# Kernel tuning notes

Hardware: AMD Instinct MI355X
Metric: run time of the kernel (lower is better)

The kernel has to match this reference:

```python
import jax, jax.numpy as jnp
import numpy as np

B, T, D, H, HS, E, K = 8, 1024, 1024, 16, 64, 8, 2
DF = 4 * D


def setup_inputs() -> dict:
    key = jax.random.key(0)
    ks = jax.random.split(key, 16)
    s = 0.02
    return {
        "x": jax.random.normal(ks[0], (B, T, D), jnp.float32),
        "noise": jax.random.normal(ks[1], (B, T, E), jnp.float32),
        # per-head attention projections, stacked over heads [H, D, HS]
        "Wq": jax.random.normal(ks[2], (H, D, HS), jnp.float32) * s,
        "Wk": jax.random.normal(ks[3], (H, D, HS), jnp.float32) * s,
        "Wv": jax.random.normal(ks[4], (H, D, HS), jnp.float32) * s,
        "Wproj": jax.random.normal(ks[5], (D, D), jnp.float32) * s,
        "bproj": jnp.zeros((D,), jnp.float32),
        "ln1_g": jnp.ones((D,), jnp.float32),
        "ln1_b": jnp.zeros((D,), jnp.float32),
        "ln2_g": jnp.ones((D,), jnp.float32),
        "ln2_b": jnp.zeros((D,), jnp.float32),
        # router
        "Wr": jax.random.normal(ks[6], (D, E), jnp.float32) * s,
        "br": jnp.zeros((E,), jnp.float32),
        "Wn": jax.random.normal(ks[7], (D, E), jnp.float32) * s,
        "bn": jnp.zeros((E,), jnp.float32),
        # experts, stacked [E, ...]
        "W1": jax.random.normal(ks[8], (E, D, DF), jnp.float32) * s,
        "b1": jnp.zeros((E, DF), jnp.float32),
        "W2": jax.random.normal(ks[9], (E, DF, D), jnp.float32) * s,
        "b2": jnp.zeros((E, D), jnp.float32),
    }


def _layernorm(x, g, b, eps=1e-5):
    mu = jnp.mean(x, axis=-1, keepdims=True)
    var = jnp.mean(jnp.square(x - mu), axis=-1, keepdims=True)
    return (x - mu) * jax.lax.rsqrt(var + eps) * g + b


def reference(x, noise, Wq, Wk, Wv, Wproj, bproj, ln1_g, ln1_b, ln2_g, ln2_b,
              Wr, br, Wn, bn, W1, b1, W2, b2):
    b_, t_, d_ = x.shape
    # ---- multi-head causal self-attention (dropout = identity, eval mode) ----
    h = _layernorm(x, ln1_g, ln1_b)
    q = jnp.einsum("btd,hdk->bhtk", h, Wq)
    k = jnp.einsum("btd,hdk->bhtk", h, Wk)
    v = jnp.einsum("btd,hdk->bhtk", h, Wv)
    # NOTE: original scales by C**-0.5 with C = n_embed (not head_size)
    score = jnp.einsum("bhqk,bhsk->bhqs", q, k) * (d_ ** -0.5)
    causal = jnp.tril(jnp.ones((t_, t_), bool))
    score = jnp.where(causal, score, -jnp.inf)
    att = jax.nn.softmax(score, axis=-1)
    o = jnp.einsum("bhqs,bhsk->bhqk", att, v)
    o = o.transpose(0, 2, 1, 3).reshape(b_, t_, d_)  # concat heads
    x = x + o @ Wproj + bproj
    # ---- noisy top-k sparse MoE ----
    h2 = _layernorm(x, ln2_g, ln2_b)
    logits = h2 @ Wr + br
    noisy_logits = logits + noise * jax.nn.softplus(h2 @ Wn + bn)
    topv, topi = jax.lax.top_k(noisy_logits, K)          # [B,T,K]
    sel = (topi[..., None] == jnp.arange(E)).any(axis=-2)  # [B,T,E] bool
    sparse = jnp.where(sel, noisy_logits, -jnp.inf)
    gate = jax.nn.softmax(sparse, axis=-1)               # zeros off top-k
    # gate[:,:,e]==0 for unselected experts, so dense sum == sparse dispatch
    moe = jnp.zeros_like(x)
    for e in range(E):
        he = jax.nn.relu(h2 @ W1[e] + b1[e]) @ W2[e] + b2[e]
        moe = moe + gate[..., e:e + 1] * he
    return x + moe
```

## Files before the change

### kernel.cpp

```cpp
#include <hip/hip_runtime.h>
#include <hip/hip_bf16.h>
#include <math.h>

#define NTOK 8192
#define DN   1024
#define HN   16
#define HSN  64
#define EN   8
#define DFN  4096
#define TN   1024
#define NQ   8388608u
#define NPB  144

typedef _Float16 f16x8 __attribute__((ext_vector_type(8)));
typedef _Float16 f16x4 __attribute__((ext_vector_type(4)));
typedef float    f32x4 __attribute__((ext_vector_type(4)));
typedef short    s16x8 __attribute__((ext_vector_type(8)));

#define MFMA_F16(A,B,C)  __builtin_amdgcn_mfma_f32_16x16x32_f16((A),(B),(C),0,0,0)
#define MFMA_BF16(A,B,C) __builtin_amdgcn_mfma_f32_16x16x32_bf16((A),(B),(C),0,0,0)

__device__ __forceinline__ unsigned short f2bf(float f){
  union { float f; unsigned u; } v; v.f = f;
  unsigned r = v.u + 0x7fffu + ((v.u >> 16) & 1u);
  return (unsigned short)(r >> 16);
}
__device__ __forceinline__ void fsplit(float v, _Float16& hi, _Float16& lo){
  hi = (_Float16)v; lo = (_Float16)(v - (float)hi);
}
__device__ __forceinline__ void gload16(const void* g, void* l){
  __builtin_amdgcn_global_load_lds((const __attribute__((address_space(1))) unsigned int*)g,
                                   (__attribute__((address_space(3))) unsigned int*)l, 16, 0, 0);
}
#define BAR() __builtin_amdgcn_s_barrier()
#define VMW_BAR(N) do { \
  asm volatile("s_waitcnt vmcnt(" #N ")" ::: "memory"); \
  __builtin_amdgcn_s_barrier(); \
} while (0)

__global__ __launch_bounds__(128) void ln1_kernel(
    const float* __restrict__ x, const float* __restrict__ g, const float* __restrict__ be,
    unsigned char* __restrict__ aph, unsigned char* __restrict__ apl)
{
  const int row = blockIdx.x;
  const int t = threadIdx.x;
  __shared__ float red[2];
  float4 va = ((const float4*)(x + (size_t)row*DN))[t*2];
  float4 vb = ((const float4*)(x + (size_t)row*DN))[t*2+1];
  float s = va.x+va.y+va.z+va.w + vb.x+vb.y+vb.z+vb.w;
  #pragma unroll
  for (int m = 32; m >= 1; m >>= 1) s += __shfl_xor(s, m);
  if ((t & 63) == 0) red[t >> 6] = s;
  __syncthreads();
  const float mu = (red[0] + red[1]) * (1.0f / DN);
  float e[8] = { va.x-mu, va.y-mu, va.z-mu, va.w-mu, vb.x-mu, vb.y-mu, vb.z-mu, vb.w-mu };
  float s2 = 0.0f;
  #pragma unroll
  for (int i = 0; i < 8; i++) s2 += e[i]*e[i];
  #pragma unroll
  for (int m = 32; m >= 1; m >>= 1) s2 += __shfl_xor(s2, m);
  __syncthreads();
  if ((t & 63) == 0) red[t >> 6] = s2;
  __syncthreads();
  const float var = (red[0] + red[1]) * (1.0f / DN);
  const float rs = 1.0f / sqrtf(var + 1e-5f);
  float4 ga = ((const float4*)g)[t*2], gb = ((const float4*)g)[t*2+1];
  float4 ba = ((const float4*)be)[t*2], bb = ((const float4*)be)[t*2+1];
  float gg[8] = { ga.x,ga.y,ga.z,ga.w, gb.x,gb.y,gb.z,gb.w };
  float bbv[8] = { ba.x,ba.y,ba.z,ba.w, bb.x,bb.y,bb.z,bb.w };
  f16x8 hi8, lo8;
  #pragma unroll
  for (int i = 0; i < 8; i++){
    _Float16 hi, lo; fsplit((e[i]*rs*gg[i] + bbv[i]) * 64.0f, hi, lo);
    hi8[i] = hi; lo8[i] = lo;
  }
  const int pb = row >> 7, r = row & 127, kt = t >> 3, kk8 = t & 7;
  size_t po = ((size_t)(pb*16 + kt))*16384 + r*128 + (size_t)((kk8 ^ (r & 7)) << 4);
  *(f16x8*)(aph + po) = hi8;
  *(f16x8*)(apl + po) = lo8;
}

__global__ __launch_bounds__(256) void wsplit_kernel(
    const float* __restrict__ Wq, const float* __restrict__ Wk, const float* __restrict__ Wv,
    const float* __restrict__ Wp,
    unsigned char* __restrict__ bqh, unsigned char* __restrict__ bql,
    unsigned char* __restrict__ bph, unsigned char* __restrict__ bpl)
{
  int b = blockIdx.x;
  const int t = threadIdx.x;
  const int r = t & 127;
  const int c0 = (t >> 7) * 4;
  if (b < 384){
    int nb = b >> 4, kt = b & 15;
    int n = nb*128 + r;
    int mat = n >> 10, h = (n >> 6) & 15, hs = n & 63;
    const float* W = (mat == 0) ? Wq : ((mat == 1) ? Wk : Wv);
    const float* src = W + (size_t)h*65536 + hs;
    unsigned char* ph = bqh + ((size_t)(nb*16 + kt))*16384 + r*128;
    unsigned char* pl = bql + ((size_t)(nb*16 + kt))*16384 + r*128;
    #pragma unroll
    for (int c = c0; c < c0 + 4; c++){
      int kk8 = c ^ (r & 7);
      f16x8 hi8, lo8;
      #pragma unroll
      for (int j = 0; j < 8; j++){
        _Float16 hi, lo; fsplit(src[(size_t)(kt*64 + kk8*8 + j)*64] * 1024.0f, hi, lo);
        hi8[j] = hi; lo8[j] = lo;
      }
      *(f16x8*)(ph + c*16) = hi8;
      *(f16x8*)(pl + c*16) = lo8;
    }
  } else {
    b -= 384;
    int nb = b >> 4, kt = b & 15;
    int n = nb*128 + r;
    unsigned char* ph = bph + ((size_t)(nb*16 + kt))*16384 + r*128;
    unsigned char* pl = bpl + ((size_t)(nb*16 + kt))*16384 + r*128;
    #pragma unroll
    for (int c = c0; c < c0 + 4; c++){
      int kk8 = c ^ (r & 7);
      f16x8 hi8, lo8;
      #pragma unroll
      for (int j = 0; j < 8; j++){
        _Float16 hi, lo; fsplit(Wp[(size_t)(kt*64 + kk8*8 + j)*DN + n] * 1024.0f, hi, lo);
        hi8[j] = hi; lo8[j] = lo;
      }
      *(f16x8*)(ph + c*16) = hi8;
      *(f16x8*)(pl + c*16) = lo8;
    }
  }
}

__global__ __launch_bounds__(256) void qkv_gemm_kernel(
    const unsigned char* __restrict__ aph, const unsigned char* __restrict__ apl,
    const unsigned char* __restrict__ bqh, const unsigned char* __restrict__ bql,
    _Float16* __restrict__ qkvout)
{
  const int mb = blockIdx.x;
  const int nb = blockIdx.y;
  __shared__ __align__(16) unsigned char As[16384], Bs[16384];
  const int t = threadIdx.x, w = t >> 6, lane = t & 63, lg = lane >> 4, lr = lane & 15;
  const int wr = w >> 1, wc = w & 1;
  f32x4 acc[4][4] = {};
  for (int kp = 0; kp < 48; kp++){
    const int ktl = kp & 15, phse = kp >> 4;
    if (w < 2){
      const unsigned char* srcA = (phse == 1 ? apl : aph) + ((size_t)(mb*16 + ktl))*16384;
      const unsigned char* s2 = srcA + w*8192 + lane*16;
      unsigned char* d = As + w*8192;
      #pragma unroll
      for (int j = 0; j < 8; j++) gload16(s2 + j*1024, d + j*1024);
    } else {
      const unsigned char* srcB = (phse == 2 ? bql : bqh) + ((size_t)(nb*16 + ktl))*16384;
      const unsigned char* s2 = srcB + (w - 2)*8192 + lane*16;
      unsigned char* d = Bs + (w - 2)*8192;
      #pragma unroll
      for (int j = 0; j < 8; j++) gload16(s2 + j*1024, d + j*1024);
    }
    __syncthreads();
    #pragma unroll
    for (int ks = 0; ks < 2; ks++){
      f16x8 a[4], bfr[4];
      #pragma unroll
      for (int f = 0; f < 4; f++){
        int ra = wr*64 + f*16 + lr;
        a[f] = *(const f16x8*)(As + ra*128 + ((ks*64 + lg*16) ^ ((ra & 7) << 4)));
      }
      #pragma unroll
      for (int f = 0; f < 4; f++){
        int rb = wc*64 + f*16 + lr;
        bfr[f] = *(const f16x8*)(Bs + rb*128 + ((ks*64 + lg*16) ^ ((rb & 7) << 4)));
      }
      #pragma unroll
      for (int fm = 0; fm < 4; fm++)
      #pragma unroll
      for (int fn = 0; fn < 4; fn++)
        acc[fm][fn] = MFMA_F16(a[fm], bfr[fn], acc[fm][fn]);
    }
    __syncthreads();
  }
  #pragma unroll
  for (int fm = 0; fm < 4; fm++)
  #pragma unroll
  for (int fn = 0; fn < 4; fn++)
  #pragma unroll
  for (int rr = 0; rr < 4; rr++){
    int m = mb*128 + wr*64 + fm*16 + lg*4 + rr;
    int n = nb*128 + wc*64 + fn*16 + lr;
    int mat = n >> 10, h = (n >> 6) & 15, hs = n & 63;
    int bb = m >> 10, tt = m & 1023;
    _Float16* dsthi = qkvout + (size_t)mat * 2u * NQ;
    _Float16* dstlo = dsthi + NQ;
    size_t oi = (((size_t)(bb*HN + h))*TN + tt)*HSN + hs;
    _Float16 hi, lo; fsplit(acc[fm][fn][rr] * (1.0f/1024.0f), hi, lo);
    dsthi[oi] = hi; dstlo[oi] = lo;
  }
}

__global__ __launch_bounds__(256) void attn_kernel(
    const _Float16* __restrict__ qkv,
    _Float16* __restrict__ ohi_, _Float16* __restrict__ olo_)
{
  const _Float16* qhi = qkv;
  const _Float16* qlo = qkv + NQ;
  const _Float16* khi = qkv + 2u*NQ;
  const _Float16* klo = qkv + 3u*NQ;
  const _Float16* vhi = qkv + 4u*NQ;
  const _Float16* vlo = qkv + 5u*NQ;
  const int qt = blockIdx.x;
  const int bh = blockIdx.y;
  const size_t base = (size_t)bh * TN * HSN;
  const int t = threadIdx.x, wid = t >> 6, lane = t & 63, lg = lane >> 4, lr = lane & 15;
  __shared__ _Float16 Khi[64][72], Klo[64][72], Vthi[64][72], Vtlo[64][72], Phi[64][72], Plo[64][72];
  f16x8 qh[2], ql[2];
  {
    const int qrow = qt*64 + wid*16 + lr;
    const _Float16* qp  = qhi + base + (size_t)qrow*HSN;
    const _Float16* qpl = qlo + base + (size_t)qrow*HSN;
    #pragma unroll
    for (int c = 0; c < 2; c++){
      qh[c] = *(const f16x8*)(qp  + c*32 + lg*8);
      ql[c] = *(const f16x8*)(qpl + c*32 + lg*8);
    }
  }
  f32x4 oacc[4] = {};
  float mrow[4], lsum[4];
  #pragma unroll
  for (int r = 0; r < 4; r++){ mrow[r] = -INFINITY; lsum[r] = 0.0f; }
  const int sr = t >> 2, sc = (t & 3) * 16;
  const float sscale = 1.0f / (4096.0f * 32.0f);
  for (int kvt = 0; kvt <= qt; kvt++){
    {
      const size_t gr = base + (size_t)(kvt*64 + sr)*HSN + sc;
      *(f16x8*)&Khi[sr][sc]     = *(const f16x8*)(khi + gr);
      *(f16x8*)&Khi[sr][sc + 8] = *(const f16x8*)(khi + gr + 8);
      *(f16x8*)&Klo[sr][sc]     = *(const f16x8*)(klo + gr);
      *(f16x8*)&Klo[sr][sc + 8] = *(const f16x8*)(klo + gr + 8);
      f16x8 v0 = *(const f16x8*)(vhi + gr), v1 = *(const f16x8*)(vhi + gr + 8);
      f16x8 w0 = *(const f16x8*)(vlo + gr), w1 = *(const f16x8*)(vlo + gr + 8);
      #pragma unroll
      for (int j = 0; j < 8; j++){
        Vthi[sc + j][sr] = v0[j]; Vthi[sc + 8 + j][sr] = v1[j];
        Vtlo[sc + j][sr] = w0[j]; Vtlo[sc + 8 + j][sr] = w1[j];
      }
    }
    __syncthreads();
    f32x4 sacc[4] = {};
    #pragma unroll
    for (int c = 0; c < 2; c++)
    #pragma unroll
    for (int fn = 0; fn < 4; fn++){
      f16x8 kh = *(const f16x8*)&Khi[fn*16 + lr][c*32 + lg*8];
      f16x8 kl = *(const f16x8*)&Klo[fn*16 + lr][c*32 + lg*8];
      sacc[fn] = MFMA_F16(qh[c], kh, sacc[fn]);
      sacc[fn] = MFMA_F16(qh[c], kl, sacc[fn]);
      sacc[fn] = MFMA_F16(ql[c], kh, sacc[fn]);
    }
    float sv[4][4], pmax[4];
    #pragma unroll
    for (int r = 0; r < 4; r++) pmax[r] = -INFINITY;
    const int qg0 = qt*64 + wid*16 + lg*4;
    #pragma unroll
    for (int fn = 0; fn < 4; fn++)
    #pragma unroll
    for (int r = 0; r < 4; r++){
      float xv = sacc[fn][r] * sscale;
      int kvg = kvt*64 + fn*16 + lr;
      xv = (kvg <= qg0 + r) ? xv : -INFINITY;
      sv[fn][r] = xv;
      pmax[r] = fmaxf(pmax[r], xv);
    }
    #pragma unroll
    for (int r = 0; r < 4; r++){
      #pragma unroll
      for (int m = 1; m < 16; m <<= 1) pmax[r] = fmaxf(pmax[r], __shfl_xor(pmax[r], m));
    }
    float alpha[4], mnew[4], psum[4];
    #pragma unroll
    for (int r = 0; r < 4; r++){
      mnew[r] = fmaxf(mrow[r], pmax[r]);
      alpha[r] = __expf(mrow[r] - mnew[r]);
      psum[r] = 0.0f;
    }
    #pragma unroll
    for (int fn = 0; fn < 4; fn++)
    #pragma unroll
    for (int r = 0; r < 4; r++){
      float p = __expf(sv[fn][r] - mnew[r]);
      psum[r] += p;
      _Float16 hi, lo; fsplit(p * 512.0f, hi, lo);
      Phi[wid*16 + lg*4 + r][fn*16 + lr] = hi;
      Plo[wid*16 + lg*4 + r][fn*16 + lr] = lo;
    }
    #pragma unroll
    for (int r = 0; r < 4; r++){
      #pragma unroll
      for (int m = 1; m < 16; m <<= 1) psum[r] += __shfl_xor(psum[r], m);
      lsum[r] = lsum[r]*alpha[r] + psum[r];
      mrow[r] = mnew[r];
    }
    #pragma unroll
    for (int fn = 0; fn < 4; fn++)
    #pragma unroll
    for (int r = 0; r < 4; r++) oacc[fn][r] *= alpha[r];
    #pragma unroll
    for (int c2 = 0; c2 < 2; c2++){
      f16x8 ph = *(const f16x8*)&Phi[wid*16 + lr][c2*32 + lg*8];
      f16x8 pl = *(const f16x8*)&Plo[wid*16 + lr][c2*32 + lg*8];
      #pragma unroll
      for (int fn = 0; fn < 4; fn++){
        f16x8 vh = *(const f16x8*)&Vthi[fn*16 + lr][c2*32 + lg*8];
        f16x8 vl = *(const f16x8*)&Vtlo[fn*16 + lr][c2*32 + lg*8];
        oacc[fn] = MFMA_F16(ph, vh, oacc[fn]);
        oacc[fn] = MFMA_F16(ph, vl, oacc[fn]);
        oacc[fn] = MFMA_F16(pl, vh, oacc[fn]);
      }
    }
    __syncthreads();
  }
  const int bb = bh >> 4, hh = bh & 15;
  #pragma unroll
  for (int fn = 0; fn < 4; fn++)
  #pragma unroll
  for (int r = 0; r < 4; r++){
    float ov = oacc[fn][r] / (32768.0f * lsum[r]);
    int m = qt*64 + wid*16 + lg*4 + r;
    size_t oi = ((size_t)(bb*TN + m))*DN + hh*HSN + fn*16 + lr;
    _Float16 hi, lo; fsplit(ov * 64.0f, hi, lo);
    ohi_[oi] = hi; olo_[oi] = lo;
  }
}

__global__ __launch_bounds__(256) void proj_gemm_kernel(
    const _Float16* __restrict__ ohi, const _Float16* __restrict__ olo,
    const unsigned char* __restrict__ bph, const unsigned char* __restrict__ bpl,
    const float* __restrict__ x, const float* __restrict__ bproj,
    float* __restrict__ out)
{
  const int mb = blockIdx.x;
  const int nb = blockIdx.y;
  __shared__ __align__(16) unsigned char As[16384], Bs[16384];
  const int t = threadIdx.x, w = t >> 6, lane = t & 63, lg = lane >> 4, lr = lane & 15;
  const int wr = w >> 1, wc = w & 1;
  f32x4 acc[4][4] = {};
  for (int kp = 0; kp < 48; kp++){
    const int ktl = kp & 15, phse = kp >> 4;
    if (w < 2){
      const _Float16* basep = (phse == 1 ? olo : ohi);
      const int rA = w*64 + (lane >> 3);
      const int c = lane & 7;
      unsigned char* d = As + w*8192;
      #pragma unroll
      for (int j = 0; j < 8; j++){
        int r = rA + j*8;
        const unsigned char* s2 = (const unsigned char*)(basep + (size_t)(mb*128 + r)*DN)
                                  + ktl*128 + ((c ^ (r & 7)) << 4);
        gload16(s2, d + j*1024);
      }
    } else {
      const unsigned char* srcB = (phse == 2 ? bpl : bph) + ((size_t)(nb*16 + ktl))*16384;
      const unsigned char* s2 = srcB + (w - 2)*8192 + lane*16;
      unsigned char* d = Bs + (w - 2)*8192;
      #pragma unroll
      for (int j = 0; j < 8; j++) gload16(s2 + j*1024, d + j*1024);
    }
    __syncthreads();
    #pragma unroll
    for (int ks = 0; ks < 2; ks++){
      f16x8 a[4], bfr[4];
      #pragma unroll
      for (int f = 0; f < 4; f++){
        int ra = wr*64 + f*16 + lr;
        a[f] = *(const f16x8*)(As + ra*128 + ((ks*64 + lg*16) ^ ((ra & 7) << 4)));
      }
      #pragma unroll
      for (int f = 0; f < 4; f++){
        int rb = wc*64 + f*16 + lr;
        bfr[f] = *(const f16x8*)(Bs + rb*128 + ((ks*64 + lg*16) ^ ((rb & 7) << 4)));
      }
      #pragma unroll
      for (int fm = 0; fm < 4; fm++)
      #pragma unroll
      for (int fn = 0; fn < 4; fn++)
        acc[fm][fn] = MFMA_F16(a[fm], bfr[fn], acc[fm][fn]);
    }
    __syncthreads();
  }
  #pragma unroll
  for (int fm = 0; fm < 4; fm++)
  #pragma unroll
  for (int fn = 0; fn < 4; fn++)
  #pragma unroll
  for (int rr = 0; rr < 4; rr++){
    int m = mb*128 + wr*64 + fm*16 + lg*4 + rr;
    int n = nb*128 + wc*64 + fn*16 + lr;
    size_t oi = (size_t)m*DN + n;
    out[oi] = x[oi] + acc[fm][fn][rr] * (1.0f/65536.0f) + bproj[n];
  }
}

__global__ __launch_bounds__(256) void router_kernel(
    const float* __restrict__ x1, const float* __restrict__ g, const float* __restrict__ be,
    const float* __restrict__ Wr, const float* __restrict__ br,
    const float* __restrict__ Wn, const float* __restrict__ bn,
    const float* __restrict__ noise, unsigned short* __restrict__ h2bf,
    int* __restrict__ topk_e, float* __restrict__ topk_g, int* __restrict__ counts)
{
  const int token = blockIdx.x;
  const int t = threadIdx.x;
  __shared__ float redsum[4];
  __shared__ float red[64];
  float4 v = ((const float4*)(x1 + (size_t)token * DN))[t];
  float s = v.x + v.y + v.z + v.w;
  #pragma unroll
  for (int m = 32; m >= 1; m >>= 1) s += __shfl_xor(s, m);
  if ((t & 63) == 0) redsum[t >> 6] = s;
  __syncthreads();
  const float mu = (redsum[0] + redsum[1] + redsum[2] + redsum[3]) * (1.0f / DN);
  const float d0 = v.x - mu, d1 = v.y - mu, d2 = v.z - mu, d3 = v.w - mu;
  float s2 = d0*d0 + d1*d1 + d2*d2 + d3*d3;
  #pragma unroll
  for (int m = 32; m >= 1; m >>= 1) s2 += __shfl_xor(s2, m);
  __syncthreads();
  if ((t & 63) == 0) redsum[t >> 6] = s2;
  __syncthreads();
  const float var = (redsum[0] + redsum[1] + redsum[2] + redsum[3]) * (1.0f / DN);
  const float rs = 1.0f / sqrtf(var + 1e-5f);
  float4 gv = ((const float4*)g)[t];
  float4 bv = ((const float4*)be)[t];
  float h0 = d0*rs*gv.x + bv.x, h1v = d1*rs*gv.y + bv.y, h2v = d2*rs*gv.z + bv.z, h3 = d3*rs*gv.w + bv.w;
  ushort4 hb;
  hb.x = f2bf(h0); hb.y = f2bf(h1v); hb.z = f2bf(h2v); hb.w = f2bf(h3);
  *(ushort4*)(h2bf + (size_t)token*DN + t*4) = hb;
  float acc[16];
  const int j = t * 4;
  #pragma unroll
  for (int e = 0; e < 8; e++){
    acc[e]     = h0*Wr[(j+0)*8+e] + h1v*Wr[(j+1)*8+e] + h2v*Wr[(j+2)*8+e] + h3*Wr[(j+3)*8+e];
    acc[8 + e] = h0*Wn[(j+0)*8+e] + h1v*Wn[(j+1)*8+e] + h2v*Wn[(j+2)*8+e] + h3*Wn[(j+3)*8+e];
  }
  #pragma unroll
  for (int q = 0; q < 16; q++){
    #pragma unroll
    for (int m = 32; m >= 1; m >>= 1) acc[q] += __shfl_xor(acc[q], m);
  }
  if ((t & 63) == 0){
    #pragma unroll
    for (int q = 0; q < 16; q++) red[(t >> 6)*16 + q] = acc[q];
  }
  __syncthreads();
  if (t < 16) red[t] = red[t] + red[16 + t] + red[32 + t] + red[48 + t];
  __syncthreads();
  if (t == 0){
    float nz[8];
    #pragma unroll
    for (int e = 0; e < 8; e++){
      float logit = red[e] + br[e];
      float a = red[8 + e] + bn[e];
      float sp = (a > 20.0f) ? a : log1pf(expf(a));
      nz[e] = logit + noise[(size_t)token*EN + e] * sp;
    }
    float v1 = -INFINITY, v2 = -INFINITY; int i1 = 0, i2 = 0;
    #pragma unroll
    for (int e = 0; e < 8; e++){
      float z = nz[e];
      if (z > v1){ v2 = v1; i2 = i1; v1 = z; i1 = e; }
      else if (z > v2){ v2 = z; i2 = e; }
    }
    float e2 = expf(v2 - v1);
    float den = 1.0f + e2;
    topk_e[token*2]     = i1; topk_e[token*2 + 1] = i2;
    topk_g[token*2]     = 1.0f/den; topk_g[token*2 + 1] = e2/den;
    atomicAdd(&counts[i1], 1); atomicAdd(&counts[i2], 1);
  }
}

__global__ void scan_kernel(const int* __restrict__ counts, int* __restrict__ offs)
{
  if (threadIdx.x == 0 && blockIdx.x == 0){
    int a = 0;
    for (int e = 0; e < EN; e++){ offs[e] = a; a += (counts[e] + 255) & ~255; }
  }
}

__global__ __launch_bounds__(256) void scatter_kernel(
    const int* __restrict__ topk_e, const float* __restrict__ topk_g,
    const int* __restrict__ offs, int* __restrict__ fill,
    int* __restrict__ rows, float* __restrict__ grow)
{
  const int token = blockIdx.x*256 + threadIdx.x;
  #pragma unroll
  for (int i = 0; i < 2; i++){
    int e = topk_e[token*2 + i];
    int pos = offs[e] + atomicAdd(&fill[e], 1);
    rows[pos] = token;
    grow[pos] = topk_g[token*2 + i];
  }
}

__global__ __launch_bounds__(256) void wconv_kernel(
    const float* __restrict__ W1, const float* __restrict__ W2,
    unsigned char* __restrict__ w1p, unsigned char* __restrict__ w2p)
{
  int b = blockIdx.x;
  const float* W; unsigned char* pan; int Nd, kt, n;
  if (b < 2048){
    int e = b >> 8, rem = b & 255, nb2 = rem >> 4; kt = rem & 15;
    n = nb2*256 + threadIdx.x;
    W = W1 + (size_t)e * DN * DFN; Nd = DFN;
    pan = w1p + (((size_t)e*32 + (n >> 7))*16 + kt) * 16384;
  } else {
    b -= 2048;
    int e = b >> 8, rem = b & 255, nb2 = rem >> 6; kt = rem & 63;
    n = nb2*256 + threadIdx.x;
    W = W2 + (size_t)e * DFN * DN; Nd = DN;
    pan = w2p + (((size_t)e*8 + (n >> 7))*64 + kt) * 16384;
  }
  const int r = n & 127;
  #pragma unroll
  for (int kk8 = 0; kk8 < 8; kk8++){
    union { unsigned short u[8]; uint4 v; } buf;
    #pragma unroll
    for (int j = 0; j < 8; j++)
      buf.u[j] = f2bf(W[(size_t)(kt*64 + kk8*8 + j)*Nd + n]);
    *(uint4*)(pan + r*128 + ((kk8 ^ (r & 7)) << 4)) = buf.v;
  }
}

__global__ __launch_bounds__(256) void agather_kernel(
    const unsigned short* __restrict__ h2bf, const int* __restrict__ rows,
    unsigned char* __restrict__ apnl)
{
  const int pb = blockIdx.x, kt = blockIdx.y;
  const int t = threadIdx.x;
  const int r = t >> 1, c0 = (t & 1) * 4;
  const int tok = rows[pb*128 + r];
  const unsigned char* src = (const unsigned char*)h2bf + (size_t)tok*2048 + kt*128;
  unsigned char* dst = apnl + ((size_t)pb*16 + kt)*16384 + r*128;
  #pragma unroll
  for (int i = 0; i < 4; i++){
    int c = c0 + i;
    *(uint4*)(dst + ((c ^ (r & 7)) << 4)) = *(const uint4*)(src + c*16);
  }
}

__global__ __launch_bounds__(512, 1) void moe1_kernel(
    const unsigned char* __restrict__ apnl, const unsigned char* __restrict__ w1p,
    const float* __restrict__ b1,
    const int* __restrict__ counts, const int* __restrict__ offs,
    unsigned short* __restrict__ midP)
{
  __shared__ __align__(16) unsigned char As[2][32768], Bs[2][32768];
  const int bid = blockIdx.x;
  const int t = threadIdx.x;
  const int w = t >> 6, lane = t & 63, lg = lane >> 4, lr = lane & 15;
  const int wm = w >> 2, wn = w & 3;
  const int sp = (w >> 1) & 1, sh = (w & 1) * 8192;
  const int e  = bid & 7;
  const int c  = bid >> 3;
  const int cnt = counts[e];
  const int off = offs[e];
  const int nmb = (cnt + 255) >> 8;
  const int nch = nmb * 16;
  for (int q = c; q < nch; q += 32){
    const int grp = q / (4*nmb);
    const int within = q - grp*4*nmb;
    const int mb = within >> 2;
    const int nb = grp*4 + (within & 3);
    const int m0 = mb * 256;
    const int pb0 = (off + m0) >> 7;
    const unsigned char* sbase;
    unsigned char* dbase;
    if (w < 4){
      sbase = apnl + ((size_t)(pb0 + sp) * 16) * 16384 + sh + lane*16;
      dbase = &As[0][sp*16384 + sh];
    } else {
      sbase = w1p + ((size_t)(e*32 + nb*2 + sp) * 16) * 16384 + sh + lane*16;
      dbase = &Bs[0][sp*16384 + sh];
    }
    f32x4 acc[8][4] = {};
    auto stage = [&](int buf, int kt){
      const unsigned char* s2 = sbase + (size_t)kt * 16384;
      unsigned char* d = dbase + buf * 32768;
      #pragma unroll
      for (int j = 0; j < 8; j++) gload16(s2 + j*1024, d + j*1024);
    };
    auto compute = [&](int buf){
      const unsigned char* pA = &As[buf][wm*16384];
      const unsigned char* pB = &Bs[buf][(wn>>1)*16384];
      #pragma unroll
      for (int ks = 0; ks < 2; ks++){
        s16x8 b[4], a[8];
        #pragma unroll
        for (int f = 0; f < 4; f++){
          int rb = (wn&1)*64 + f*16 + lr;
          b[f] = *(const s16x8*)(pB + rb*128 + ((ks*64 + lg*16) ^ ((rb&7)<<4)));
        }
        #pragma unroll
        for (int f = 0; f < 8; f++){
          int ra = f*16 + lr;
          a[f] = *(const s16x8*)(pA + ra*128 + ((ks*64 + lg*16) ^ ((ra&7)<<4)));
        }
        __builtin_amdgcn_s_setprio(1);
        #pragma unroll
        for (int fm = 0; fm < 8; fm++)
        #pragma unroll
        for (int fn = 0; fn < 4; fn++)
          acc[fm][fn] = MFMA_BF16(a[fm], b[fn], acc[fm][fn]);
        __builtin_amdgcn_s_setprio(0);
      }
    };
    stage(0, 0);
    stage(1, 1);
    for (int kt = 0; kt + 2 < 16; kt += 2){
      VMW_BAR(8); compute(0); BAR(); stage(0, kt + 2);
      VMW_BAR(8); compute(1); BAR(); stage(1, kt + 3);
    }
    VMW_BAR(8); compute(0);
    VMW_BAR(0); compute(1);
    BAR();
    {
      unsigned char* Lp = ((wm == 0) ? (unsigned char*)As : (unsigned char*)Bs) + wn*16384;
      const float* b1e = b1 + (size_t)e*DFN + nb*256 + wn*64;
      #pragma unroll
      for (int fn = 0; fn < 4; fn++){
        float bias = b1e[fn*16 + lr];
        int col = fn*16 + lr;
        #pragma unroll
        for (int fm = 0; fm < 8; fm++)
        #pragma unroll
        for (int rr = 0; rr < 4; rr++){
          int r = fm*16 + lg*4 + rr;
          float v = fmaxf(acc[fm][fn][rr] + bias, 0.0f);
          *(unsigned short*)(Lp + r*128 + ((col ^ ((r & 7) << 3)) * 2)) = f2bf(v);
        }
      }
    }
    BAR();
    {
      int p = w >> 2, jj = w & 3;
      const uint4* src = (const uint4*)(((p == 0) ? (unsigned char*)As : (unsigned char*)Bs) + jj*16384);
      uint4* dst = (uint4*)((unsigned char*)midP + (((size_t)(pb0 + p)*64) + nb*4 + jj) * 16384);
      #pragma unroll
      for (int i = 0; i < 16; i++) dst[lane + i*64] = src[lane + i*64];
    }
    BAR();
  }
}

__global__ __launch_bounds__(512, 1) void moe2_kernel(
    const unsigned char* __restrict__ midP, const unsigned char* __restrict__ w2p,
    const float* __restrict__ b2,
    const int* __restrict__ counts, const int* __restrict__ offs,
    const int* __restrict__ rows, const float* __restrict__ grow,
    float* __restrict__ out)
{
  __shared__ __align__(16) unsigned char As[2][32768], Bs[2][32768];
  const int bid = blockIdx.x;
  const int t = threadIdx.x;
  const int w = t >> 6, lane = t & 63, lg = lane >> 4, lr = lane & 15;
  const int wm = w >> 2, wn = w & 3;
  const int sp = (w >> 1) & 1, sh = (w & 1) * 8192;
  const int e  = bid & 7;
  const int c  = bid >> 3;
  const int cnt = counts[e];
  const int off = offs[e];
  const int nmb = (cnt + 255) >> 8;
  const int nch = nmb * 4;
  for (int q = c; q < nch; q += 32){
    const int mb = q >> 2;
    const int nb = q & 3;
    const int m0 = mb * 256;
    const int pb0 = (off + m0) >> 7;
    const unsigned char* sbase;
    unsigned char* dbase;
    if (w < 4){
      sbase = midP + ((size_t)(pb0 + sp) * 64) * 16384 + sh + lane*16;
      dbase = &As[0][sp*16384 + sh];
    } else {
      sbase = w2p + ((size_t)(e*8 + nb*2 + sp) * 64) * 16384 + sh + lane*16;
      dbase = &Bs[0][sp*16384 + sh];
    }
    f32x4 acc[8][4] = {};
    auto stage = [&](int buf, int kt){
      const unsigned char* s2 = sbase + (size_t)kt * 16384;
      unsigned char* d = dbase + buf * 32768;
      #pragma unroll
      for (int j = 0; j < 8; j++) gload16(s2 + j*1024, d + j*1024);
    };
    auto compute = [&](int buf){
      const unsigned char* pA = &As[buf][wm*16384];
      const unsigned char* pB = &Bs[buf][(wn>>1)*16384];
      #pragma unroll
      for (int ks = 0; ks < 2; ks++){
        s16x8 b[4], a[8];
        #pragma unroll
        for (int f = 0; f < 4; f++){
          int rb = (wn&1)*64 + f*16 + lr;
          b[f] = *(const s16x8*)(pB + rb*128 + ((ks*64 + lg*16) ^ ((rb&7)<<4)));
        }
        #pragma unroll
        for (int f = 0; f < 8; f++){
          int ra = f*16 + lr;
          a[f] = *(const s16x8*)(pA + ra*128 + ((ks*64 + lg*16) ^ ((ra&7)<<4)));
        }
        __builtin_amdgcn_s_setprio(1);
        #pragma unroll
        for (int fm = 0; fm < 8; fm++)
        #pragma unroll
        for (int fn = 0; fn < 4; fn++)
          acc[fm][fn] = MFMA_BF16(a[fm], b[fn], acc[fm][fn]);
        __builtin_amdgcn_s_setprio(0);
      }
    };
    stage(0, 0);
    stage(1, 1);
    for (int kt = 0; kt + 2 < 64; kt += 2){
      VMW_BAR(8); compute(0); BAR(); stage(0, kt + 2);
      VMW_BAR(8); compute(1); BAR(); stage(1, kt + 3);
    }
    VMW_BAR(8); compute(0);
    VMW_BAR(0); compute(1);
    BAR();
    const float* b2e = b2 + (size_t)e*DN + nb*256 + wn*64;
    #pragma unroll
    for (int fm = 0; fm < 8; fm++)
    #pragma unroll
    for (int rr = 0; rr < 4; rr++){
      int ml = wm*128 + fm*16 + lg*4 + rr;
      if (m0 + ml < cnt){
        int gi = off + m0 + ml;
        int tok = rows[gi];
        float gt = grow[gi];
        #pragma unroll
        for (int fn = 0; fn < 4; fn++){
          int n = nb*256 + wn*64 + fn*16 + lr;
          atomicAdd(out + (size_t)tok*DN + n, gt*(acc[fm][fn][rr] + b2e[fn*16 + lr]));
        }
      }
    }
  }
}

extern "C" void kernel_launch(void* const* d_in, const int* in_sizes, int n_in,
                              void* d_out, int out_size, void* d_ws, size_t ws_size,
                              hipStream_t stream) {
  (void)in_sizes; (void)n_in; (void)out_size; (void)ws_size;
  const float* x     = (const float*)d_in[0];
  const float* noise = (const float*)d_in[1];
  const float* Wq    = (const float*)d_in[2];
  const float* Wk    = (const float*)d_in[3];
  const float* Wv    = (const float*)d_in[4];
  const float* Wp    = (const float*)d_in[5];
  const float* bproj = (const float*)d_in[6];
  const float* ln1g  = (const float*)d_in[7];
  const float* ln1b  = (const float*)d_in[8];
  const float* ln2g  = (const float*)d_in[9];
  const float* ln2b  = (const float*)d_in[10];
  const float* Wr    = (const float*)d_in[11];
  const float* br    = (const float*)d_in[12];
  const float* Wn    = (const float*)d_in[13];
  const float* bn    = (const float*)d_in[14];
  const float* W1    = (const float*)d_in[15];
  const float* b1    = (const float*)d_in[16];
  const float* W2    = (const float*)d_in[17];
  const float* b2    = (const float*)d_in[18];
  float* out = (float*)d_out;

  char* w = (char*)d_ws;
  auto alloc = [&](size_t bytes) -> char* {
    char* p = w; w += (bytes + 255) & ~(size_t)255; return p;
  };
  char* big = alloc((size_t)NPB * 64 * 16384);
  _Float16* qkvsplit = (_Float16*)big;
  _Float16* ohi = (_Float16*)(big + (size_t)6*NQ*2);
  _Float16* olo = ohi + NQ;
  unsigned short* midP = (unsigned short*)big;
  char* attn_tmp = w;
  unsigned char* aph = (unsigned char*)alloc((size_t)64*16*16384);
  unsigned char* apl = (unsigned char*)alloc((size_t)64*16*16384);
  unsigned char* bqh = (unsigned char*)alloc((size_t)24*16*16384);
  unsigned char* bql = (unsigned char*)alloc((size_t)24*16*16384);
  unsigned char* bph = (unsigned char*)alloc((size_t)8*16*16384);
  unsigned char* bpl = (unsigned char*)alloc((size_t)8*16*16384);
  unsigned char* w1p = (unsigned char*)attn_tmp;
  char* w1p_end = attn_tmp + (size_t)EN*DFN*DN*2;
  if (w < w1p_end) w = w1p_end;
  unsigned char* w2p = (unsigned char*)alloc((size_t)EN*DN*DFN*2);
  unsigned char* apnl = (unsigned char*)alloc((size_t)NPB*16*16384);
  unsigned short* h2bf = (unsigned short*)alloc((size_t)NTOK*DN*2);
  int*   topk_e = (int*)alloc(NTOK*2*sizeof(int));
  float* topk_g = (float*)alloc(NTOK*2*sizeof(float));
  int*   rowsA  = (int*)alloc((size_t)NPB*128*sizeof(int));
  float* growA  = (float*)alloc((size_t)NPB*128*sizeof(float));
  int*   cnts   = (int*)alloc(256);
  int*   fill   = cnts + 8;
  int*   offs   = cnts + 16;

  (void)hipMemsetAsync(cnts, 0, 64, stream);
  (void)hipMemsetAsync(rowsA, 0, (size_t)NPB*128*sizeof(int), stream);
  ln1_kernel<<<NTOK, 128, 0, stream>>>(x, ln1g, ln1b, aph, apl);
  wsplit_kernel<<<512, 256, 0, stream>>>(Wq, Wk, Wv, Wp, bqh, bql, bph, bpl);
  qkv_gemm_kernel<<<dim3(64, 24), 256, 0, stream>>>(aph, apl, bqh, bql, qkvsplit);
  attn_kernel<<<dim3(16, 128), 256, 0, stream>>>(qkvsplit, ohi, olo);
  proj_gemm_kernel<<<dim3(64, 8), 256, 0, stream>>>(ohi, olo, bph, bpl, x, bproj, out);
  wconv_kernel<<<4096, 256, 0, stream>>>(W1, W2, w1p, w2p);
  router_kernel<<<NTOK, 256, 0, stream>>>(out, ln2g, ln2b, Wr, br, Wn, bn, noise,
                                          h2bf, topk_e, topk_g, cnts);
  scan_kernel<<<1, 64, 0, stream>>>(cnts, offs);
  scatter_kernel<<<NTOK/256, 256, 0, stream>>>(topk_e, topk_g, offs, fill, rowsA, growA);
  agather_kernel<<<dim3(NPB, 16), 256, 0, stream>>>(h2bf, rowsA, apnl);
  moe1_kernel<<<256, 512, 0, stream>>>(apnl, w1p, b1, cnts, offs, midP);
  moe2_kernel<<<256, 512, 0, stream>>>((const unsigned char*)midP, w2p, b2,
                                       cnts, offs, rowsA, growA, out);
}
```

Measured before the change: 1.531 ms.

## Use atomic work queue, split-K moe2, single-buffer LDS for higher occupancy

Replaces the static per-expert block assignment in both MoE GEMMs with a global atomic work counter over a flattened task list built in the scan kernel, so experts with uneven token counts are load-balanced. moe2 is split into four K-chunks, each accumulated via atomics, with the bias added only by the first chunk. LDS is cut from double to single buffering so more blocks can be resident (launch bounds 512,4, grid 512). This gives up the async prefetch overlap, since loads now complete before compute within each k-step, and it adds more output atomics.

```diff
diff --git a/kernel.cpp b/kernel.cpp
--- a/kernel.cpp
+++ b/kernel.cpp
@@ -32,11 +32,6 @@
   __builtin_amdgcn_global_load_lds((const __attribute__((address_space(1))) unsigned int*)g,
                                    (__attribute__((address_space(3))) unsigned int*)l, 16, 0, 0);
 }
-#define BAR() __builtin_amdgcn_s_barrier()
-#define VMW_BAR(N) do { \
-  asm volatile("s_waitcnt vmcnt(" #N ")" ::: "memory"); \
-  __builtin_amdgcn_s_barrier(); \
-} while (0)
 
 __global__ __launch_bounds__(128) void ln1_kernel(
     const float* __restrict__ x, const float* __restrict__ g, const float* __restrict__ be,
@@ -475,11 +470,19 @@
   }
 }
 
-__global__ void scan_kernel(const int* __restrict__ counts, int* __restrict__ offs)
+__global__ void scan_kernel(const int* __restrict__ counts, int* __restrict__ offs,
+                            int* __restrict__ qmeta)
 {
   if (threadIdx.x == 0 && blockIdx.x == 0){
-    int a = 0;
-    for (int e = 0; e < EN; e++){ offs[e] = a; a += (counts[e] + 255) & ~255; }
+    int a = 0, t1 = 0, t2 = 0;
+    for (int e = 0; e < EN; e++){
+      offs[e] = a; a += (counts[e] + 255) & ~255;
+      int nmb = (counts[e] + 255) >> 8;
+      qmeta[e] = t1;      t1 += nmb * 16;
+      qmeta[16 + e] = t2; t2 += nmb * 16;
+    }
+    qmeta[8] = t1;
+    qmeta[24] = t2;
   }
 }
 
@@ -544,27 +547,34 @@
   }
 }
 
-__global__ __launch_bounds__(512, 1) void moe1_kernel(
+__global__ __launch_bounds__(512, 4) void moe1_kernel(
     const unsigned char* __restrict__ apnl, const unsigned char* __restrict__ w1p,
     const float* __restrict__ b1,
     const int* __restrict__ counts, const int* __restrict__ offs,
+    const int* __restrict__ qmeta, int* __restrict__ ctr,
     unsigned short* __restrict__ midP)
 {
-  __shared__ __align__(16) unsigned char As[2][32768], Bs[2][32768];
-  const int bid = blockIdx.x;
+  __shared__ __align__(16) unsigned char As[32768], Bs[32768];
+  __shared__ int qs;
   const int t = threadIdx.x;
   const int w = t >> 6, lane = t & 63, lg = lane >> 4, lr = lane & 15;
   const int wm = w >> 2, wn = w & 3;
   const int sp = (w >> 1) & 1, sh = (w & 1) * 8192;
-  const int e  = bid & 7;
-  const int c  = bid >> 3;
-  const int cnt = counts[e];
-  const int off = offs[e];
-  const int nmb = (cnt + 255) >> 8;
-  const int nch = nmb * 16;
-  for (int q = c; q < nch; q += 32){
-    const int grp = q / (4*nmb);
-    const int within = q - grp*4*nmb;
+  const int T = qmeta[8];
+  for (;;){
+    __syncthreads();
+    if (t == 0) qs = atomicAdd(ctr, 1);
+    __syncthreads();
+    const int q = qs;
+    if (q >= T) break;
+    int e = 0;
+    #pragma unroll
+    for (int i = 1; i < 8; i++) if (q >= qmeta[i]) e = i;
+    const int local = q - qmeta[e];
+    const int cnt = counts[e], off = offs[e];
+    const int nmb = (cnt + 255) >> 8;
+    const int grp = local / (4*nmb);
+    const int within = local - grp*4*nmb;
     const int mb = within >> 2;
     const int nb = grp*4 + (within & 3);
     const int m0 = mb * 256;
@@ -573,21 +583,19 @@
     unsigned char* dbase;
     if (w < 4){
       sbase = apnl + ((size_t)(pb0 + sp) * 16) * 16384 + sh + lane*16;
-      dbase = &As[0][sp*16384 + sh];
+      dbase = As + sp*16384 + sh;
     } else {
       sbase = w1p + ((size_t)(e*32 + nb*2 + sp) * 16) * 16384 + sh + lane*16;
-      dbase = &Bs[0][sp*16384 + sh];
+      dbase = Bs + sp*16384 + sh;
     }
     f32x4 acc[8][4] = {};
-    auto stage = [&](int buf, int kt){
+    for (int kt = 0; kt < 16; kt++){
       const unsigned char* s2 = sbase + (size_t)kt * 16384;
-      unsigned char* d = dbase + buf * 32768;
-      #pragma unroll
-      for (int j = 0; j < 8; j++) gload16(s2 + j*1024, d + j*1024);
-    };
-    auto compute = [&](int buf){
-      const unsigned char* pA = &As[buf][wm*16384];
-      const unsigned char* pB = &Bs[buf][(wn>>1)*16384];
+      #pragma unroll
+      for (int j = 0; j < 8; j++) gload16(s2 + j*1024, dbase + j*1024);
+      __syncthreads();
+      const unsigned char* pA = As + wm*16384;
+      const unsigned char* pB = Bs + (wn>>1)*16384;
       #pragma unroll
       for (int ks = 0; ks < 2; ks++){
         s16x8 b[4], a[8];
@@ -609,88 +617,89 @@
           acc[fm][fn] = MFMA_BF16(a[fm], b[fn], acc[fm][fn]);
         __builtin_amdgcn_s_setprio(0);
       }
-    };
-    stage(0, 0);
-    stage(1, 1);
-    for (int kt = 0; kt + 2 < 16; kt += 2){
-      VMW_BAR(8); compute(0); BAR(); stage(0, kt + 2);
-      VMW_BAR(8); compute(1); BAR(); stage(1, kt + 3);
-    }
-    VMW_BAR(8); compute(0);
-    VMW_BAR(0); compute(1);
-    BAR();
-    {
-      unsigned char* Lp = ((wm == 0) ? (unsigned char*)As : (unsigned char*)Bs) + wn*16384;
-      const float* b1e = b1 + (size_t)e*DFN + nb*256 + wn*64;
-      #pragma unroll
-      for (int fn = 0; fn < 4; fn++){
-        float bias = b1e[fn*16 + lr];
-        int col = fn*16 + lr;
-        #pragma unroll
-        for (int fm = 0; fm < 8; fm++)
-        #pragma unroll
-        for (int rr = 0; rr < 4; rr++){
-          int r = fm*16 + lg*4 + rr;
-          float v = fmaxf(acc[fm][fn][rr] + bias, 0.0f);
-          *(unsigned short*)(Lp + r*128 + ((col ^ ((r & 7) << 3)) * 2)) = f2bf(v);
+      __syncthreads();
+    }
+    #pragma unroll
+    for (int p = 0; p < 2; p++){
+      if (wm == p){
+        unsigned char* Lp = (wn < 2) ? (As + wn*16384) : (Bs + (wn-2)*16384);
+        const float* b1e = b1 + (size_t)e*DFN + nb*256 + wn*64;
+        #pragma unroll
+        for (int fn = 0; fn < 4; fn++){
+          float bias = b1e[fn*16 + lr];
+          int col = fn*16 + lr;
+          #pragma unroll
+          for (int fm = 0; fm < 8; fm++)
+          #pragma unroll
+          for (int rr = 0; rr < 4; rr++){
+            int r = fm*16 + lg*4 + rr;
+            float v = fmaxf(acc[fm][fn][rr] + bias, 0.0f);
+            *(unsigned short*)(Lp + r*128 + ((col ^ ((r & 7) << 3)) * 2)) = f2bf(v);
+          }
         }
       }
-    }
-    BAR();
-    {
-      int p = w >> 2, jj = w & 3;
-      const uint4* src = (const uint4*)(((p == 0) ? (unsigned char*)As : (unsigned char*)Bs) + jj*16384);
-      uint4* dst = (uint4*)((unsigned char*)midP + (((size_t)(pb0 + p)*64) + nb*4 + jj) * 16384);
-      #pragma unroll
-      for (int i = 0; i < 16; i++) dst[lane + i*64] = src[lane + i*64];
-    }
-    BAR();
-  }
-}
-
-__global__ __launch_bounds__(512, 1) void moe2_kernel(
+      __syncthreads();
+      {
+        int panel = w >> 1, half = w & 1;
+        const uint4* src = (const uint4*)(((panel < 2) ? (As + panel*16384) : (Bs + (panel-2)*16384)) + half*8192);
+        uint4* dst = (uint4*)((unsigned char*)midP + (((size_t)(pb0 + p)*64) + nb*4 + panel)*16384 + half*8192);
+        #pragma unroll
+        for (int i = 0; i < 8; i++) dst[lane + i*64] = src[lane + i*64];
+      }
+      __syncthreads();
+    }
+  }
+}
+
+__global__ __launch_bounds__(512, 4) void moe2_kernel(
     const unsigned char* __restrict__ midP, const unsigned char* __restrict__ w2p,
     const float* __restrict__ b2,
     const int* __restrict__ counts, const int* __restrict__ offs,
+    const int* __restrict__ qmeta, int* __restrict__ ctr,
     const int* __restrict__ rows, const float* __restrict__ grow,
     float* __restrict__ out)
 {
-  __shared__ __align__(16) unsigned char As[2][32768], Bs[2][32768];
-  const int bid = blockIdx.x;
+  __shared__ __align__(16) unsigned char As[32768], Bs[32768];
+  __shared__ int qs;
   const int t = threadIdx.x;
   const int w = t >> 6, lane = t & 63, lg = lane >> 4, lr = lane & 15;
   const int wm = w >> 2, wn = w & 3;
   const int sp = (w >> 1) & 1, sh = (w & 1) * 8192;
-  const int e  = bid & 7;
-  const int c  = bid >> 3;
-  const int cnt = counts[e];
-  const int off = offs[e];
-  const int nmb = (cnt + 255) >> 8;
-  const int nch = nmb * 4;
-  for (int q = c; q < nch; q += 32){
-    const int mb = q >> 2;
-    const int nb = q & 3;
+  const int T = qmeta[24];
+  for (;;){
+    __syncthreads();
+    if (t == 0) qs = atomicAdd(ctr, 1);
+    __syncthreads();
+    const int q = qs;
+    if (q >= T) break;
+    int e = 0;
+    #pragma unroll
+    for (int i = 1; i < 8; i++) if (q >= qmeta[16 + i]) e = i;
+    const int local = q - qmeta[16 + e];
+    const int cnt = counts[e], off = offs[e];
+    const int nb = local & 3;
+    const int r2 = local >> 2;
+    const int kh = r2 & 3;
+    const int mb = r2 >> 2;
     const int m0 = mb * 256;
     const int pb0 = (off + m0) >> 7;
     const unsigned char* sbase;
     unsigned char* dbase;
     if (w < 4){
-      sbase = midP + ((size_t)(pb0 + sp) * 64) * 16384 + sh + lane*16;
-      dbase = &As[0][sp*16384 + sh];
+      sbase = midP + (((size_t)(pb0 + sp))*64 + kh*16)*16384 + sh + lane*16;
+      dbase = As + sp*16384 + sh;
     } else {
-      sbase = w2p + ((size_t)(e*8 + nb*2 + sp) * 64) * 16384 + sh + lane*16;
-      dbase = &Bs[0][sp*16384 + sh];
+      sbase = w2p + (((size_t)(e*8 + nb*2 + sp))*64 + kh*16)*16384 + sh + lane*16;
+      dbase = Bs + sp*16384 + sh;
     }
     f32x4 acc[8][4] = {};
-    auto stage = [&](int buf, int kt){
+    for (int kt = 0; kt < 16; kt++){
       const unsigned char* s2 = sbase + (size_t)kt * 16384;
-      unsigned char* d = dbase + buf * 32768;
-      #pragma unroll
-      for (int j = 0; j < 8; j++) gload16(s2 + j*1024, d + j*1024);
-    };
-    auto compute = [&](int buf){
-      const unsigned char* pA = &As[buf][wm*16384];
-      const unsigned char* pB = &Bs[buf][(wn>>1)*16384];
+      #pragma unroll
+      for (int j = 0; j < 8; j++) gload16(s2 + j*1024, dbase + j*1024);
+      __syncthreads();
+      const unsigned char* pA = As + wm*16384;
+      const unsigned char* pB = Bs + (wn>>1)*16384;
       #pragma unroll
       for (int ks = 0; ks < 2; ks++){
         s16x8 b[4], a[8];
@@ -712,16 +721,8 @@
           acc[fm][fn] = MFMA_BF16(a[fm], b[fn], acc[fm][fn]);
         __builtin_amdgcn_s_setprio(0);
       }
-    };
-    stage(0, 0);
-    stage(1, 1);
-    for (int kt = 0; kt + 2 < 64; kt += 2){
-      VMW_BAR(8); compute(0); BAR(); stage(0, kt + 2);
-      VMW_BAR(8); compute(1); BAR(); stage(1, kt + 3);
-    }
-    VMW_BAR(8); compute(0);
-    VMW_BAR(0); compute(1);
-    BAR();
+      __syncthreads();
+    }
     const float* b2e = b2 + (size_t)e*DN + nb*256 + wn*64;
     #pragma unroll
     for (int fm = 0; fm < 8; fm++)
@@ -735,7 +736,8 @@
         #pragma unroll
         for (int fn = 0; fn < 4; fn++){
           int n = nb*256 + wn*64 + fn*16 + lr;
-          atomicAdd(out + (size_t)tok*DN + n, gt*(acc[fm][fn][rr] + b2e[fn*16 + lr]));
+          float bias = (kh == 0) ? b2e[fn*16 + lr] : 0.0f;
+          atomicAdd(out + (size_t)tok*DN + n, gt*(acc[fm][fn][rr] + bias));
         }
       }
     }
@@ -796,8 +798,11 @@
   int*   cnts   = (int*)alloc(256);
   int*   fill   = cnts + 8;
   int*   offs   = cnts + 16;
-
-  (void)hipMemsetAsync(cnts, 0, 64, stream);
+  int*   ctr1   = cnts + 24;
+  int*   ctr2   = cnts + 25;
+  int*   qmeta  = (int*)alloc(128);
+
+  (void)hipMemsetAsync(cnts, 0, 128, stream);
   (void)hipMemsetAsync(rowsA, 0, (size_t)NPB*128*sizeof(int), stream);
   ln1_kernel<<<NTOK, 128, 0, stream>>>(x, ln1g, ln1b, aph, apl);
   wsplit_kernel<<<512, 256, 0, stream>>>(Wq, Wk, Wv, Wp, bqh, bql, bph, bpl);
@@ -807,10 +812,10 @@
   wconv_kernel<<<4096, 256, 0, stream>>>(W1, W2, w1p, w2p);
   router_kernel<<<NTOK, 256, 0, stream>>>(out, ln2g, ln2b, Wr, br, Wn, bn, noise,
                                           h2bf, topk_e, topk_g, cnts);
-  scan_kernel<<<1, 64, 0, stream>>>(cnts, offs);
+  scan_kernel<<<1, 64, 0, stream>>>(cnts, offs, qmeta);
   scatter_kernel<<<NTOK/256, 256, 0, stream>>>(topk_e, topk_g, offs, fill, rowsA, growA);
   agather_kernel<<<dim3(NPB, 16), 256, 0, stream>>>(h2bf, rowsA, apnl);
-  moe1_kernel<<<256, 512, 0, stream>>>(apnl, w1p, b1, cnts, offs, midP);
-  moe2_kernel<<<256, 512, 0, stream>>>((const unsigned char*)midP, w2p, b2,
-                                       cnts, offs, rowsA, growA, out);
-}
+  moe1_kernel<<<512, 512, 0, stream>>>(apnl, w1p, b1, cnts, offs, qmeta, ctr1, midP);
+  moe2_kernel<<<512, 512, 0, stream>>>((const unsigned char*)midP, w2p, b2,
+                                       cnts, offs, qmeta, ctr2, rowsA, growA, out);
+}
```

After: 4.573 ms. +198.7%, slower.
